# Performance work log

Measured on AMD Instinct MI355X. Metric: run time of the kernel, lower is better.

Reference implementation:

```python
import math
import jax, jax.numpy as jnp
import numpy as np

B, T, C, H = 4, 2048, 1024, 16
D = C // H  # head dim = 64


def setup_inputs() -> dict:
    key = jax.random.key(0)
    k1, k2, k3 = jax.random.split(key, 3)
    scale = 1.0 / math.sqrt(C)
    return {
        "x": jax.random.normal(k1, (B, T, C), jnp.float32),
        "w_attn": jax.random.normal(k2, (C, 3 * C), jnp.float32) * scale,
        "b_attn": jnp.zeros((3 * C,), jnp.float32),
        "w_proj": jax.random.normal(k3, (C, C), jnp.float32) * scale,
        "b_proj": jnp.zeros((C,), jnp.float32),
    }


def reference(x, w_attn, b_attn, w_proj, b_proj):
    Bx, Tx, Cx = x.shape
    qkv = x @ w_attn + b_attn                       # [B,T,3C]
    q, k, v = jnp.split(qkv, 3, axis=-1)
    # [B,T,C] -> [B,H,T,D]
    q = q.reshape(Bx, Tx, H, D).transpose(0, 2, 1, 3)
    k = k.reshape(Bx, Tx, H, D).transpose(0, 2, 1, 3)
    v = v.reshape(Bx, Tx, H, D).transpose(0, 2, 1, 3)
    att = jnp.einsum('bhqd,bhkd->bhqk', q, k) * (1.0 / math.sqrt(D))
    causal = jnp.tril(jnp.ones((Tx, Tx), bool))     # [T,T]
    att = jnp.where(causal, att, -jnp.inf)
    att = jax.nn.softmax(att, axis=-1)
    y = jnp.einsum('bhqk,bhkd->bhqd', att, v)       # [B,H,T,D]
    y = y.transpose(0, 2, 1, 3).reshape(Bx, Tx, Cx)
    return y @ w_proj + b_proj
```

## Files before the change

kernel.cpp:

```cpp
#include <hip/hip_runtime.h>
#include <hip/hip_bf16.h>

typedef __bf16 bf16;
typedef __attribute__((ext_vector_type(4))) __bf16 bf16x4;
typedef __attribute__((ext_vector_type(8))) __bf16 bf16x8;
typedef __attribute__((ext_vector_type(4))) float f32x4;
typedef __attribute__((ext_vector_type(16))) float f32x16;
typedef __attribute__((ext_vector_type(2))) unsigned u32x2;
typedef __attribute__((ext_vector_type(4))) unsigned u32x4;

#define B_ 4
#define T_ 2048
#define C_ 1024
#define H_ 16
#define D_ 64
#define BT_ (B_*T_)

#define NEG_INF (-__builtin_inff())

__device__ __forceinline__ void gld16(const void* g, void* l) {
  __builtin_amdgcn_global_load_lds(
      (const __attribute__((address_space(1))) void*)g,
      (__attribute__((address_space(3))) void*)l, 16, 0, 0);
}

__device__ __forceinline__ unsigned cvtpk(float lo, float hi) {
  unsigned r;
  asm("v_cvt_pk_bf16_f32 %0, %1, %2" : "=v"(r) : "v"(lo), "v"(hi));
  return r;
}


__global__ void cast_x(const float* __restrict__ in, bf16* __restrict__ out) {
  int i = blockIdx.x * 256 + threadIdx.x;
  f32x4 v = reinterpret_cast<const f32x4*>(in)[i];
  bf16x4 o;
  o[0] = (bf16)v[0]; o[1] = (bf16)v[1]; o[2] = (bf16)v[2]; o[3] = (bf16)v[3];
  reinterpret_cast<bf16x4*>(out)[i] = o;
}

__global__ void transpose_cast(const float* __restrict__ in, bf16* __restrict__ out,
                               int R, int Cc) {
  __shared__ float tile[32][33];
  int tx = threadIdx.x, ty = threadIdx.y;
  int x  = blockIdx.x * 32 + tx;
  int y0 = blockIdx.y * 32;
#pragma unroll
  for (int j = 0; j < 32; j += 8)
    tile[ty + j][tx] = in[(size_t)(y0 + ty + j) * Cc + x];
  __syncthreads();
  int ox  = y0 + tx;
  int oy0 = blockIdx.x * 32;
#pragma unroll
  for (int j = 0; j < 32; j += 8)
    out[(size_t)(oy0 + ty + j) * R + ox] = (bf16)tile[tx][ty + j];
}


template<int EPI>
__global__ __launch_bounds__(512, 4)
void gemm_bt(const bf16* __restrict__ A, const bf16* __restrict__ Bt,
             const float* __restrict__ bias, float* __restrict__ outF,
             bf16* __restrict__ qb, bf16* __restrict__ kb, bf16* __restrict__ vb,
             int M, int N, int K) {
  __shared__ alignas(16) bf16 As[3][128 * 32];
  __shared__ alignas(16) bf16 Bs[3][256 * 32];
  const int tid = threadIdx.x;
  const int lane = tid & 63, wid = tid >> 6;
  const int wm = wid >> 2, wn = wid & 3;
  const int lr = lane & 15, lg = lane >> 4;
  const int fx = (lr ^ (lr >> 2)) & 3;
  const int koff = (lg ^ fx) << 3;

  const int nbx = gridDim.x;
  const int bid = blockIdx.y * nbx + blockIdx.x;
  const int x = bid & 7, j = bid >> 3;
  const int mpx = gridDim.y >> 3;
  const int m0 = (x * mpx + j % mpx) * 128;
  const int n0 = (j / mpx) * 256;

  f32x4 acc[4][4] = {};

#define GSTAGE(BF, KT) do {                                                    \
    int k0_ = (KT) << 5;                                                       \
    { int row_ = tid >> 2, sl_ = tid & 3;                                      \
      int gs_ = sl_ ^ ((row_ ^ (row_ >> 2)) & 3);                              \
      gld16(A + (size_t)(m0 + row_) * K + k0_ + (gs_ << 3), As[BF] + tid * 8); }\
    _Pragma("unroll")                                                          \
    for (int j_ = 0; j_ < 2; ++j_) {                                           \
      int s_ = j_ * 512 + tid;                                                 \
      int row_ = s_ >> 2, sl_ = s_ & 3;                                        \
      int gs_ = sl_ ^ ((row_ ^ (row_ >> 2)) & 3);                              \
      gld16(Bt + (size_t)(n0 + row_) * K + k0_ + (gs_ << 3), Bs[BF] + s_ * 8); \
    }                                                                          \
  } while (0)

  const int ktiles = K >> 5;
  GSTAGE(0, 0);
  GSTAGE(1, 1);
  for (int kt = 0; kt < ktiles; ++kt) {
    if (kt + 1 < ktiles) asm volatile("s_waitcnt vmcnt(3)" ::: "memory");
    else                 asm volatile("s_waitcnt vmcnt(0)" ::: "memory");
    __builtin_amdgcn_s_barrier();
    asm volatile("" ::: "memory");
    if (kt + 2 < ktiles) GSTAGE((kt + 2) % 3, kt + 2);

    const bf16* Ac = As[kt % 3];
    const bf16* Bc = Bs[kt % 3];
    bf16x8 af[4], bfr[4];
#pragma unroll
    for (int i = 0; i < 4; i++)
      af[i]  = *(const bf16x8*)(Ac + ((wm * 64 + i * 16 + lr) << 5) + koff);
#pragma unroll
    for (int j2 = 0; j2 < 4; j2++)
      bfr[j2] = *(const bf16x8*)(Bc + ((wn * 64 + j2 * 16 + lr) << 5) + koff);
    __builtin_amdgcn_s_setprio(1);
#pragma unroll
    for (int i = 0; i < 4; i++)
#pragma unroll
      for (int j2 = 0; j2 < 4; j2++)
        acc[i][j2] = __builtin_amdgcn_mfma_f32_16x16x32_bf16(af[i], bfr[j2], acc[i][j2], 0, 0, 0);
    __builtin_amdgcn_s_setprio(0);
  }
#undef GSTAGE

  if (EPI == 1) {
#pragma unroll
    for (int i = 0; i < 4; i++) {
      int row = m0 + wm * 64 + i * 16 + lg * 4;
#pragma unroll
      for (int j2 = 0; j2 < 4; j2++) {
        int col = n0 + wn * 64 + j2 * 16 + lr;
        float bv = bias[col];
#pragma unroll
        for (int r = 0; r < 4; r++)
          outF[(size_t)(row + r) * N + col] = acc[i][j2][r] + bv;
      }
    }
  } else {
    const int sect = n0 >> 10;
#pragma unroll
    for (int i = 0; i < 4; i++) {
      int row = m0 + wm * 64 + i * 16 + lg * 4;
#pragma unroll
      for (int j2 = 0; j2 < 4; j2++) {
        int col = n0 + wn * 64 + j2 * 16 + lr;
        float bv = bias[col];
        int cm = col & 1023;
        int h = cm >> 6, d = cm & 63;
#pragma unroll
        for (int r = 0; r < 4; r++) {
          float v = acc[i][j2][r] + bv;
          int rt = row + r;
          int b = rt >> 11, t = rt & 2047;
          bf16 o = (bf16)v;
          size_t bh = (size_t)(b * H_ + h);
          if (sect == 0)      qb[(bh * T_ + t) * D_ + d] = o;
          else if (sect == 1) kb[(bh * T_ + t) * D_ + d] = o;
          else                vb[(bh * D_ + d) * T_ + t] = o;
        }
      }
    }
  }
}


#if __has_builtin(__builtin_amdgcn_permlane32_swap)
#define PERMSWAP(A, B, LOW, HIW) do {                                           \
    auto _r = __builtin_amdgcn_permlane32_swap((unsigned)(A), (unsigned)(B),    \
                                               false, false);                   \
    __builtin_memcpy(&(LOW), &_r, 4);                                           \
    __builtin_memcpy(&(HIW), (const char*)&_r + 4, 4);                          \
  } while (0)
#else
#define PERMSWAP(A, B, LOW, HIW) do {                                           \
    unsigned _sb = (unsigned)__shfl_xor((int)(B), 32, 64);                      \
    unsigned _sa = (unsigned)__shfl_xor((int)(A), 32, 64);                      \
    (LOW) = hi ? _sb : (A);                                                     \
    (HIW) = hi ? (B) : _sa;                                                     \
  } while (0)
#endif

__global__ __launch_bounds__(256, 4)
void attn_fwd(const bf16* __restrict__ qg, const bf16* __restrict__ kg,
              const bf16* __restrict__ vg, bf16* __restrict__ yb) {
  __shared__ alignas(16) bf16 Ks[3][64 * 64];
  __shared__ alignas(16) bf16 Vs[3][64 * 64];
  const int tid = threadIdx.x;
  const int lane = tid & 63, wid = tid >> 6;
  const int hi = lane >> 5, lq = lane & 31;
  const int xr = (lq & 7) << 4;
  const int bh = blockIdx.y;
  const int NQ = T_ / 128;

  const char* kbase = (const char*)(kg + (size_t)bh * T_ * D_);
  const char* vbase = (const char*)(vg + (size_t)bh * D_ * T_);
  const int b_ = bh >> 4, h = bh & 15;

#define STAGE(BF, TT) do {                                                     \
    _Pragma("unroll")                                                          \
    for (int j_ = 0; j_ < 2; ++j_) {                                           \
      int s_ = j_ * 256 + tid;                                                 \
      int row_ = s_ >> 3;                                                      \
      int scb_ = ((s_ & 7) << 4) ^ ((row_ & 7) << 4);                          \
      gld16(kbase + (size_t)((TT) * 64 + row_) * 128 + scb_,                   \
            (char*)Ks[BF] + s_ * 16);                                          \
      gld16(vbase + (size_t)row_ * (T_ * 2) + (TT) * 128 + scb_,               \
            (char*)Vs[BF] + s_ * 16);                                          \
    }                                                                          \
  } while (0)

  for (int ph = 0; ph < 2; ++ph) {
    const int qblk = ph ? (int)blockIdx.x : (NQ - 1 - (int)blockIdx.x);
    const int wq0 = qblk * 128 + wid * 32;
    const int qrow = wq0 + lq;
    const int nt = 2 * qblk + 2;

    if (ph) __builtin_amdgcn_s_barrier();
    STAGE(0, 0);
    STAGE(1, 1);

    const bf16* qptr = qg + ((size_t)bh * T_ + qrow) * D_ + hi * 8;
    bf16x8 qf[4];
#pragma unroll
    for (int s = 0; s < 4; s++) {
      qf[s] = *(const bf16x8*)(qptr + 16 * s);
      asm volatile("" : "+v"(qf[s]));
    }

    f32x16 o[2] = {};
    float mrow = NEG_INF, lrow = 0.f;

    for (int t = 0; t < nt; ++t) {
      if (t + 1 < nt) asm volatile("s_waitcnt vmcnt(4)" ::: "memory");
      else            asm volatile("s_waitcnt vmcnt(0)" ::: "memory");
      __builtin_amdgcn_s_barrier();
      asm volatile("" ::: "memory");
      if (t + 2 < nt) STAGE((t + 2) % 3, t + 2);

      const char* Kc = (const char*)Ks[t % 3];
      const char* Vc = (const char*)Vs[t % 3];

      f32x16 S[2] = {};
      __builtin_amdgcn_s_setprio(1);
#pragma unroll
      for (int s = 0; s < 4; s++) {
#pragma unroll
        for (int b = 0; b < 2; b++) {
          bf16x8 kf = *(const bf16x8*)(Kc + (b * 32 + lq) * 128 +
                                       ((32 * s + 16 * hi) ^ xr));
          S[b] = __builtin_amdgcn_mfma_f32_32x32x16_bf16(kf, qf[s], S[b], 0, 0, 0);
        }
      }
      __builtin_amdgcn_s_setprio(0);

      if (t >= nt - 2) {
#pragma unroll
        for (int b = 0; b < 2; b++)
#pragma unroll
          for (int r = 0; r < 16; r++) {
            int kgl = t * 64 + b * 32 + (r & 3) + 8 * (r >> 2) + 4 * hi;
            if (kgl > qrow) S[b][r] = NEG_INF;
          }
      }

      float tm = NEG_INF;
#pragma unroll
      for (int b = 0; b < 2; b++)
#pragma unroll
        for (int r = 0; r < 16; r++) tm = fmaxf(tm, S[b][r]);
      tm = fmaxf(tm, __shfl_xor(tm, 32, 64));

      float mn = fmaxf(mrow, 0.125f * tm);
      float alpha = __expf(mrow - mn);
      mrow = mn;
      float rs = 0.f;
#pragma unroll
      for (int b = 0; b < 2; b++)
#pragma unroll
        for (int r = 0; r < 16; r++) {
          float e = __expf(fmaf(S[b][r], 0.125f, -mn));
          S[b][r] = e;
          rs += e;
        }
      rs += __shfl_xor(rs, 32, 64);
      lrow = lrow * alpha + rs;
#pragma unroll
      for (int db = 0; db < 2; db++)
#pragma unroll
        for (int r = 0; r < 16; r++) o[db][r] *= alpha;

      __builtin_amdgcn_s_setprio(1);
#pragma unroll
      for (int ks = 0; ks < 4; ks++) {
        const int b = ks >> 1, hf = ks & 1;
        unsigned A0 = cvtpk(S[b][8 * hf + 0], S[b][8 * hf + 1]);
        unsigned A1 = cvtpk(S[b][8 * hf + 2], S[b][8 * hf + 3]);
        unsigned B0 = cvtpk(S[b][8 * hf + 4], S[b][8 * hf + 5]);
        unsigned B1 = cvtpk(S[b][8 * hf + 6], S[b][8 * hf + 7]);
        unsigned w0, w1, w2, w3;
        PERMSWAP(A0, B0, w0, w2);
        PERMSWAP(A1, B1, w1, w3);
        u32x4 wv = {w0, w1, w2, w3};
        bf16x8 pf = __builtin_bit_cast(bf16x8, wv);
#pragma unroll
        for (int db = 0; db < 2; db++) {
          bf16x8 vf = *(const bf16x8*)(Vc + (db * 32 + lq) * 128 +
                                       ((32 * ks + 16 * hi) ^ xr));
          o[db] = __builtin_amdgcn_mfma_f32_32x32x16_bf16(vf, pf, o[db], 0, 0, 0);
        }
      }
      __builtin_amdgcn_s_setprio(0);
    }

    float inv = 1.f / lrow;
    bf16* yrow = yb + ((size_t)(b_ * T_ + qrow)) * C_ + h * 64 + hi * 4;
#pragma unroll
    for (int db = 0; db < 2; db++)
#pragma unroll
      for (int rq = 0; rq < 4; rq++) {
        unsigned w0 = cvtpk(o[db][4 * rq + 0] * inv, o[db][4 * rq + 1] * inv);
        unsigned w1 = cvtpk(o[db][4 * rq + 2] * inv, o[db][4 * rq + 3] * inv);
        u32x2 wv = {w0, w1};
        *(u32x2*)(yrow + db * 32 + rq * 8) = wv;
      }
  }
#undef STAGE
}


extern "C" void kernel_launch(void* const* d_in, const int* in_sizes, int n_in,
                              void* d_out, int out_size, void* d_ws, size_t ws_size,
                              hipStream_t stream) {
  (void)in_sizes; (void)n_in; (void)out_size; (void)ws_size;
  const float* x      = (const float*)d_in[0];
  const float* w_attn = (const float*)d_in[1];
  const float* b_attn = (const float*)d_in[2];
  const float* w_proj = (const float*)d_in[3];
  const float* b_proj = (const float*)d_in[4];
  float* out = (float*)d_out;

  char* ws = (char*)d_ws;
  bf16* x_bf = (bf16*)ws;  ws += (size_t)BT_ * C_ * 2;
  bf16* wat  = (bf16*)ws;  ws += (size_t)3 * C_ * C_ * 2;
  bf16* wpt  = (bf16*)ws;  ws += (size_t)C_ * C_ * 2;
  bf16* qbuf = (bf16*)ws;  ws += (size_t)BT_ * C_ * 2;
  bf16* kbuf = (bf16*)ws;  ws += (size_t)BT_ * C_ * 2;
  bf16* vbuf = (bf16*)ws;  ws += (size_t)BT_ * C_ * 2;
  bf16* ybuf = (bf16*)ws;

  cast_x<<<(BT_ * C_ / 4) / 256, 256, 0, stream>>>(x, x_bf);
  transpose_cast<<<dim3(3 * C_ / 32, C_ / 32), dim3(32, 8), 0, stream>>>(w_attn, wat, C_, 3 * C_);
  transpose_cast<<<dim3(C_ / 32, C_ / 32), dim3(32, 8), 0, stream>>>(w_proj, wpt, C_, C_);

  gemm_bt<0><<<dim3(3 * C_ / 256, BT_ / 128), 512, 0, stream>>>(
      x_bf, wat, b_attn, nullptr, qbuf, kbuf, vbuf, BT_, 3 * C_, C_);

  attn_fwd<<<dim3(T_ / 256, B_ * H_), 256, 0, stream>>>(qbuf, kbuf, vbuf, ybuf);

  gemm_bt<1><<<dim3(C_ / 256, BT_ / 128), 512, 0, stream>>>(
      ybuf, wpt, b_proj, out, nullptr, nullptr, nullptr, BT_, C_, C_);
}
```

Measured before the change: 289.0 us.

## Shrink GEMM tile to 128x128 with 256 threads and double buffering

Changes the GEMM block tile from 128x256 with 8 waves and a triple-buffered LDS pipeline to 128x128 with 4 waves and double buffering. The LDS swizzle also changes to a simpler (row>>1)&3 XOR pattern. The loads for the next stage are now issued after the barrier, with a vmcnt wait placed after them. The smaller tiles give more blocks and lower LDS use, which may help occupancy and load balance, but each block does less reuse and the pipeline has less prefetch depth.

```diff
diff --git a/kernel.cpp b/kernel.cpp
--- a/kernel.cpp
+++ b/kernel.cpp
@@ -58,62 +58,70 @@
 
 
 template<int EPI>
-__global__ __launch_bounds__(512, 4)
+__global__ __launch_bounds__(256, 3)
 void gemm_bt(const bf16* __restrict__ A, const bf16* __restrict__ Bt,
              const float* __restrict__ bias, float* __restrict__ outF,
              bf16* __restrict__ qb, bf16* __restrict__ kb, bf16* __restrict__ vb,
              int M, int N, int K) {
-  __shared__ alignas(16) bf16 As[3][128 * 32];
-  __shared__ alignas(16) bf16 Bs[3][256 * 32];
+  __shared__ alignas(16) bf16 As[2][128 * 32];
+  __shared__ alignas(16) bf16 Bs[2][128 * 32];
   const int tid = threadIdx.x;
   const int lane = tid & 63, wid = tid >> 6;
-  const int wm = wid >> 2, wn = wid & 3;
+  const int wm = wid >> 1, wn = wid & 1;
   const int lr = lane & 15, lg = lane >> 4;
-  const int fx = (lr ^ (lr >> 2)) & 3;
-  const int koff = (lg ^ fx) << 3;
 
   const int nbx = gridDim.x;
   const int bid = blockIdx.y * nbx + blockIdx.x;
-  const int x = bid & 7, j = bid >> 3;
+  const int xcd = bid & 7, j = bid >> 3;
   const int mpx = gridDim.y >> 3;
-  const int m0 = (x * mpx + j % mpx) * 128;
-  const int n0 = (j / mpx) * 256;
+  const int m0 = (xcd * mpx + j % mpx) * 128;
+  const int n0 = (j / mpx) * 128;
 
   f32x4 acc[4][4] = {};
 
 #define GSTAGE(BF, KT) do {                                                    \
-    int k0_ = (KT) << 5;                                                       \
-    { int row_ = tid >> 2, sl_ = tid & 3;                                      \
-      int gs_ = sl_ ^ ((row_ ^ (row_ >> 2)) & 3);                              \
-      gld16(A + (size_t)(m0 + row_) * K + k0_ + (gs_ << 3), As[BF] + tid * 8); }\
+    const int k0_ = (KT) << 5;                                                 \
     _Pragma("unroll")                                                          \
     for (int j_ = 0; j_ < 2; ++j_) {                                           \
-      int s_ = j_ * 512 + tid;                                                 \
-      int row_ = s_ >> 2, sl_ = s_ & 3;                                        \
-      int gs_ = sl_ ^ ((row_ ^ (row_ >> 2)) & 3);                              \
-      gld16(Bt + (size_t)(n0 + row_) * K + k0_ + (gs_ << 3), Bs[BF] + s_ * 8); \
+      int S_ = j_ * 256 + tid;                                                 \
+      int row_ = S_ >> 2, sl_ = (S_ & 3) ^ ((row_ >> 1) & 3);                  \
+      gld16(A + (size_t)(m0 + row_) * K + k0_ + (sl_ << 3), As[BF] + S_ * 8);  \
+    }                                                                          \
+    _Pragma("unroll")                                                          \
+    for (int j_ = 0; j_ < 2; ++j_) {                                           \
+      int S_ = j_ * 256 + tid;                                                 \
+      int row_ = S_ >> 2, sl_ = (S_ & 3) ^ ((row_ >> 1) & 3);                  \
+      gld16(Bt + (size_t)(n0 + row_) * K + k0_ + (sl_ << 3), Bs[BF] + S_ * 8); \
     }                                                                          \
   } while (0)
 
   const int ktiles = K >> 5;
   GSTAGE(0, 0);
-  GSTAGE(1, 1);
   for (int kt = 0; kt < ktiles; ++kt) {
-    if (kt + 1 < ktiles) asm volatile("s_waitcnt vmcnt(3)" ::: "memory");
-    else                 asm volatile("s_waitcnt vmcnt(0)" ::: "memory");
     __builtin_amdgcn_s_barrier();
+    if (kt + 1 < ktiles) {
+      GSTAGE((kt + 1) & 1, kt + 1);
+      asm volatile("s_waitcnt vmcnt(4)" ::: "memory");
+    } else {
+      asm volatile("s_waitcnt vmcnt(0)" ::: "memory");
+    }
     asm volatile("" ::: "memory");
-    if (kt + 2 < ktiles) GSTAGE((kt + 2) % 3, kt + 2);
-
-    const bf16* Ac = As[kt % 3];
-    const bf16* Bc = Bs[kt % 3];
+
+    const bf16* Ac = As[kt & 1];
+    const bf16* Bc = Bs[kt & 1];
     bf16x8 af[4], bfr[4];
 #pragma unroll
-    for (int i = 0; i < 4; i++)
-      af[i]  = *(const bf16x8*)(Ac + ((wm * 64 + i * 16 + lr) << 5) + koff);
-#pragma unroll
-    for (int j2 = 0; j2 < 4; j2++)
-      bfr[j2] = *(const bf16x8*)(Bc + ((wn * 64 + j2 * 16 + lr) << 5) + koff);
+    for (int i = 0; i < 4; i++) {
+      int row = wm * 64 + i * 16 + lr;
+      int slot = lg ^ ((row >> 1) & 3);
+      af[i] = *(const bf16x8*)(Ac + (row << 5) + (slot << 3));
+    }
+#pragma unroll
+    for (int j2 = 0; j2 < 4; j2++) {
+      int row = wn * 64 + j2 * 16 + lr;
+      int slot = lg ^ ((row >> 1) & 3);
+      bfr[j2] = *(const bf16x8*)(Bc + (row << 5) + (slot << 3));
+    }
     __builtin_amdgcn_s_setprio(1);
 #pragma unroll
     for (int i = 0; i < 4; i++)
@@ -353,11 +361,11 @@
   transpose_cast<<<dim3(3 * C_ / 32, C_ / 32), dim3(32, 8), 0, stream>>>(w_attn, wat, C_, 3 * C_);
   transpose_cast<<<dim3(C_ / 32, C_ / 32), dim3(32, 8), 0, stream>>>(w_proj, wpt, C_, C_);
 
-  gemm_bt<0><<<dim3(3 * C_ / 256, BT_ / 128), 512, 0, stream>>>(
+  gemm_bt<0><<<dim3(3 * C_ / 128, BT_ / 128), 256, 0, stream>>>(
       x_bf, wat, b_attn, nullptr, qbuf, kbuf, vbuf, BT_, 3 * C_, C_);
 
   attn_fwd<<<dim3(T_ / 256, B_ * H_), 256, 0, stream>>>(qbuf, kbuf, vbuf, ybuf);
 
-  gemm_bt<1><<<dim3(C_ / 256, BT_ / 128), 512, 0, stream>>>(
+  gemm_bt<1><<<dim3(C_ / 128, BT_ / 128), 256, 0, stream>>>(
       ybuf, wpt, b_proj, out, nullptr, nullptr, nullptr, BT_, C_, C_);
 }
```

After: 273.1 us. -5.5%, faster.
